# Performance work log

Measured on AMD Instinct MI355X. Metric: run time of the kernel, lower is better.

## Reference

```python
import jax, jax.numpy as jnp
import numpy as np

PLP_ORDER = 16
N_CHANNEL = 40
FFT_LENGTH = 512
SAMPLE_RATE = 16000
LIFTER = 22
COMP_FACTOR = 0.33
FLOOR = 1e-5
F_MIN = 0.0
F_MAX = SAMPLE_RATE / 2


def _hz_to_mel(hz):
    return 1127.0 * np.log1p(np.asarray(hz, dtype=np.float64) / 700.0)


def _mel_to_hz(mel):
    return 700.0 * np.expm1(np.asarray(mel, dtype=np.float64) / 1127.0)


def _build_constants():
    # SPTK-style mel filter bank (triangular in mel domain).
    mel_min = _hz_to_mel(F_MIN)
    mel_max = _hz_to_mel(F_MAX)
    lower_bin = max(1, int(F_MIN / SAMPLE_RATE * FFT_LENGTH + 1.5))
    upper_bin = min(FFT_LENGTH // 2, int(F_MAX / SAMPLE_RATE * FFT_LENGTH + 0.5))
    seed = np.arange(1, N_CHANNEL + 2)
    cf_mel = (mel_max - mel_min) / (N_CHANNEL + 1) * seed + mel_min  # (C+1,)
    bins = np.arange(lower_bin, upper_bin)
    mel = _hz_to_mel(SAMPLE_RATE * bins / FFT_LENGTH)
    ch = np.searchsorted(cf_mel, mel, side='left')  # first center freq >= mel
    diff = cf_mel - np.concatenate([[mel_min], cf_mel[:-1]])
    w = (cf_mel[ch] - mel) / diff[ch]
    H = np.zeros((len(bins), N_CHANNEL))
    rows = np.arange(len(bins))
    low = ch - 1
    m_lo = low >= 0
    H[rows[m_lo], low[m_lo]] += w[m_lo]
    m_hi = ch <= N_CHANNEL - 1
    H[rows[m_hi], ch[m_hi]] += 1.0 - w[m_hi]
    # Equal-loudness curve over the first C center frequencies (in Hz).
    cf_hz = _mel_to_hz(cf_mel)
    f2 = cf_hz[:N_CHANNEL] ** 2
    eql = (f2 / (f2 + 160000.0)) ** 2 * (f2 + 1440000.0) / (f2 + 9610000.0)
    # Liftering vector, v[0] = 2.
    m = np.arange(PLP_ORDER + 1)
    lift = 1.0 + LIFTER / 2.0 * np.sin(np.pi / LIFTER * m)
    lift[0] = 2.0
    return lower_bin, upper_bin, H.astype(np.float32), eql.astype(np.float32), lift.astype(np.float32)


LOWER_BIN, UPPER_BIN, H_NP, EQL_NP, LIFT_NP = _build_constants()


def _levinson_durbin(r):
    # r: (..., M+1) autocorrelation -> (gain K, LPC coefficients a_1..a_M)
    M = PLP_ORDER
    E = r[..., 0]
    a = jnp.zeros(r.shape[:-1] + (M,), r.dtype)
    for i in range(1, M + 1):
        acc = r[..., i]
        if i > 1:
            acc = acc + jnp.einsum('...j,...j->...', a[..., : i - 1], r[..., 1:i][..., ::-1])
        k = -acc / E
        if i > 1:
            a = a.at[..., : i - 1].set(a[..., : i - 1] + k[..., None] * a[..., : i - 1][..., ::-1])
        a = a.at[..., i - 1].set(k)
        E = E * (1.0 - k * k)
    return jnp.sqrt(E), a


def _lpc_to_cepstrum(K, a):
    # c0 = log K; c_m = -a_m - sum_{k=1}^{m-1} (k/m) c_k a_{m-k}
    M = PLP_ORDER
    c = [jnp.log(K)]
    for m in range(1, M + 1):
        acc = a[..., m - 1]
        for k in range(1, m):
            acc = acc + (k / m) * c[k] * a[..., m - k - 1]
        c.append(-acc)
    return jnp.stack(c, axis=-1)  # (..., M+1)


def _plp(x):
    H = jnp.asarray(H_NP)
    eql = jnp.asarray(EQL_NP)
    lift = jnp.asarray(LIFT_NP)
    # Mel filter bank on power spectrum (use_power=True)
    fb = jnp.matmul(x[..., LOWER_BIN:UPPER_BIN], H)          # (..., C)
    logfb = jnp.log(jnp.maximum(fb, FLOOR))
    # Equal-loudness scaling + cubic-root amplitude compression
    y = (jnp.exp(logfb) * eql) ** COMP_FACTOR                # (..., C)
    # replicate1: duplicate first and last channels
    y = jnp.concatenate([y[..., :1], y, y[..., -1:]], axis=-1)  # (..., C+2)
    n = y.shape[-1]
    # hfft with norm='forward' -> inverse-FFT-like autocorrelation
    r = jnp.fft.hfft(y) / (2 * (n - 1))
    r = r[..., : PLP_ORDER + 1]
    K, a = _levinson_durbin(r)
    c = _lpc_to_cepstrum(K, a)
    c = c * lift
    return c[..., 1:]  # out_format 'y': PLP without C0, (..., M)


def setup_inputs() -> dict:
    key = jax.random.key(0)
    x = jax.random.uniform(key, (32, 4096, FFT_LENGTH // 2 + 1), dtype=jnp.float32)
    return {"x": x}


def reference(x):
    return _plp(x)
```

## Files before the change

### kernel.cpp

```cpp
#include <hip/hip_runtime.h>

#define NCH   40
#define MORD  16
#define NR    17
#define NY    42
#define NBINS 257

namespace cfg {

constexpr double PI  = 3.14159265358979323846264338327950288;
constexpr double LN2 = 0.693147180559945309417232121458176568;

constexpr double cexp(double x) {
    double t = 1.0, s = 1.0;
    for (int i = 1; i < 40; ++i) { t *= x / i; s += t; }
    return s;
}

constexpr double clog(double z) {
    double lg = 0.0;
    while (z > 1.4142135623730951) { z *= 0.5; lg += LN2; }
    while (z < 0.7071067811865476) { z *= 2.0; lg -= LN2; }
    double u = (z - 1.0) / (z + 1.0), u2 = u * u, t = u, s = u;
    for (int k = 1; k < 24; ++k) { t *= u2; s += t / (2.0 * k + 1.0); }
    return lg + 2.0 * s;
}

constexpr double ccos(double x) {
    double tp = 2.0 * PI;
    double q = x / tp;
    long long k = (long long)(q + (q >= 0.0 ? 0.5 : -0.5));
    double r = x - (double)k * tp;
    double r2 = r * r, t = 1.0, s = 1.0;
    for (int i = 1; i < 20; ++i) { t *= -r2 / ((2.0 * i - 1.0) * (2.0 * i)); s += t; }
    return s;
}

constexpr double csin(double x) { return ccos(x - PI / 2.0); }

struct Tab {
    int   start[43];
    float w[257];
    float eql[NCH];
    float lift[NR];
    float ct[NR][NY];
    constexpr Tab() : start(), w(), eql(), lift(), ct() {
        const double lmax  = clog(87.0 / 7.0);
        const double U1127 = lmax / 41.0;
        for (int c = 0; c <= 42 - 1; ++c) {
            double thr = 22.4 * (cexp((double)c * U1127) - 1.0);
            int s = (int)thr + 1;
            if (s < 1) s = 1;
            if (s > 256) s = 256;
            start[c] = s;
        }
        start[42 - 1] = start[41];
        for (int c = 0; c <= 40; ++c) {
            for (int b = start[c]; b < start[c + 1]; ++b) {
                double mel = 1127.0 * clog(1.0 + (double)b * 31.25 / 700.0);
                double t   = mel / (1127.0 * U1127);
                w[b] = (float)(t - (double)c);
            }
        }
        for (int c = 0; c < NCH; ++c) {
            double cf = 700.0 * (cexp((double)(c + 1) * U1127) - 1.0);
            double f2 = cf * cf;
            double e  = f2 / (f2 + 160000.0);
            e = e * e * (f2 + 1440000.0) / (f2 + 9610000.0);
            eql[c] = (float)e;
        }
        for (int m = 0; m < NR; ++m)
            lift[m] = (float)(1.0 + 11.0 * csin(PI * (double)m / 22.0));
        lift[0] = 2.0f;
        for (int l = 0; l < NR; ++l)
            for (int j = 0; j < NY; ++j) {
                double s = (j == 0 || j == NY - 1) ? 1.0 : 2.0;
                ct[l][j] = (float)(s * ccos(PI * (double)(j * l) / 41.0) / 82.0);
            }
    }
};

constexpr Tab T{};

}

__global__ __launch_bounds__(256) void plp_kernel(const float* __restrict__ x,
                                                  float* __restrict__ out,
                                                  int nframes)
{
    using cfg::T;
    const long long frame = (long long)blockIdx.x * blockDim.x + threadIdx.x;
    if (frame >= nframes) return;
    const float* __restrict__ xf = x + frame * NBINS;

    float fb[NCH];
    #pragma unroll
    for (int c = 0; c < NCH; ++c) fb[c] = 0.f;

    #pragma unroll
    for (int c = 0; c <= 40; ++c) {
        #pragma unroll
        for (int b = T.start[c]; b < T.start[c + 1]; ++b) {
            float xv = xf[b];
            const float wa = T.w[b];
            if (c < 40) fb[c]     = fmaf(wa, xv, fb[c]);
            if (c >= 1) fb[c - 1] = fmaf(1.0f - wa, xv, fb[c - 1]);
        }
    }

    float ys[NY];
    #pragma unroll
    for (int c = 0; c < NCH; ++c) {
        float v = fmaxf(fb[c], 1e-5f) * T.eql[c];
        ys[c + 1] = __expf(0.33f * __logf(v));
    }
    ys[0] = ys[1];
    ys[NY - 1] = ys[NY - 2];

    float r[NR];
    #pragma unroll
    for (int l = 0; l < NR; ++l) {
        float acc = 0.f;
        #pragma unroll
        for (int j = 0; j < NY; ++j) acc = fmaf(T.ct[l][j], ys[j], acc);
        r[l] = acc;
    }

    float a[MORD];
    #pragma unroll
    for (int i = 0; i < MORD; ++i) a[i] = 0.f;
    float E = r[0];
    #pragma unroll
    for (int i = 1; i <= MORD; ++i) {
        float acc = r[i];
        #pragma unroll
        for (int j = 0; j < i - 1; ++j) acc = fmaf(a[j], r[i - 1 - j], acc);
        float k = -acc / E;
        const int half = (i - 1) / 2;
        #pragma unroll
        for (int j = 0; j < half; ++j) {
            float t1 = a[j], t2 = a[i - 2 - j];
            a[j]         = fmaf(k, t2, t1);
            a[i - 2 - j] = fmaf(k, t1, t2);
        }
        if ((i - 1) & 1) a[half] = fmaf(k, a[half], a[half]);
        a[i - 1] = k;
        E = E * (1.f - k * k);
    }

    float cc[NR];
    #pragma unroll
    for (int m = 1; m <= MORD; ++m) {
        float acc = a[m - 1];
        #pragma unroll
        for (int k2 = 1; k2 < m; ++k2)
            acc = fmaf(((float)k2 / (float)m) * cc[k2], a[m - k2 - 1], acc);
        cc[m] = -acc;
    }

    float o[16];
    #pragma unroll
    for (int m = 1; m <= MORD; ++m) o[m - 1] = cc[m] * T.lift[m];

    float4* op = reinterpret_cast<float4*>(out + (size_t)frame * 16);
    op[0] = make_float4(o[0],  o[1],  o[2],  o[3]);
    op[1] = make_float4(o[4],  o[5],  o[6],  o[7]);
    op[2] = make_float4(o[8],  o[9],  o[10], o[11]);
    op[3] = make_float4(o[12], o[13], o[14], o[15]);
}

extern "C" void kernel_launch(void* const* d_in, const int* in_sizes, int n_in,
                              void* d_out, int out_size, void* d_ws, size_t ws_size,
                              hipStream_t stream) {
    const float* x   = (const float*)d_in[0];
    float*      outp = (float*)d_out;
    int nframes = in_sizes[0] / NBINS;
    int nblocks = (nframes + 255) / 256;
    plp_kernel<<<nblocks, 256, 0, stream>>>(x, outp, nframes);
}
```

Before: 221.3 us.

## Stage frame spectra into LDS with coalesced direct global-to-LDS loads

Each block of 64 frames now copies its contiguous 64x257-float slab into shared memory with global_load_lds 16-byte transfers, so consecutive lanes read consecutive addresses. Threads then read their own frame from LDS. Before, each thread walked its own frame with a 1028-byte stride, which gave poorly coalesced global reads. In exchange the block size drops from 256 to 64 and each block uses about 66 KB of LDS. That limits occupancy, and the per-thread LDS reads at stride 257 may hit bank conflicts.

```diff
diff --git a/kernel.cpp b/kernel.cpp
--- a/kernel.cpp
+++ b/kernel.cpp
@@ -5,6 +5,7 @@
 #define NR    17
 #define NY    42
 #define NBINS 257
+#define FPB   64
 
 namespace cfg {
 
@@ -47,7 +48,7 @@
     constexpr Tab() : start(), w(), eql(), lift(), ct() {
         const double lmax  = clog(87.0 / 7.0);
         const double U1127 = lmax / 41.0;
-        for (int c = 0; c <= 42 - 1; ++c) {
+        for (int c = 0; c <= 41; ++c) {
             double thr = 22.4 * (cexp((double)c * U1127) - 1.0);
             int s = (int)thr + 1;
             if (s < 1) s = 1;
@@ -84,14 +85,34 @@
 
 }
 
-__global__ __launch_bounds__(256) void plp_kernel(const float* __restrict__ x,
+__global__ __launch_bounds__(FPB) void plp_kernel(const float* __restrict__ x,
                                                   float* __restrict__ out,
                                                   int nframes)
 {
     using cfg::T;
-    const long long frame = (long long)blockIdx.x * blockDim.x + threadIdx.x;
+    __shared__ float slab[FPB * NBINS];
+    const int tid = threadIdx.x;
+    const long long F0 = (long long)blockIdx.x * FPB;
+
+    {
+        const float* base = x + F0 * NBINS + tid * 4;
+        const float* gend = x + (long long)nframes * NBINS;
+        #pragma unroll
+        for (int k = 0; k < 65; ++k) {
+            const int off = (k < 64) ? k * 256 : (FPB * NBINS - 256);
+            const float* src = base + off;
+            if (src + 4 > gend) src = gend - 4;
+            __builtin_amdgcn_global_load_lds(
+                (const __attribute__((address_space(1))) void*)src,
+                (__attribute__((address_space(3))) void*)(slab + off),
+                16, 0, 0);
+        }
+    }
+    __syncthreads();
+
+    const long long frame = F0 + tid;
     if (frame >= nframes) return;
-    const float* __restrict__ xf = x + frame * NBINS;
+    const float* __restrict__ fr = slab + tid * NBINS;
 
     float fb[NCH];
     #pragma unroll
@@ -101,7 +122,7 @@
     for (int c = 0; c <= 40; ++c) {
         #pragma unroll
         for (int b = T.start[c]; b < T.start[c + 1]; ++b) {
-            float xv = xf[b];
+            float xv = fr[b];
             const float wa = T.w[b];
             if (c < 40) fb[c]     = fmaf(wa, xv, fb[c]);
             if (c >= 1) fb[c - 1] = fmaf(1.0f - wa, xv, fb[c - 1]);
@@ -175,6 +196,6 @@
     const float* x   = (const float*)d_in[0];
     float*      outp = (float*)d_out;
     int nframes = in_sizes[0] / NBINS;
-    int nblocks = (nframes + 255) / 256;
-    plp_kernel<<<nblocks, 256, 0, stream>>>(x, outp, nframes);
-}
+    int nblocks = (nframes + FPB - 1) / FPB;
+    plp_kernel<<<nblocks, FPB, 0, stream>>>(x, outp, nframes);
+}
```

After: 204.6 us. -7.6%, faster.

## Stage frame slabs through LDS with coalesced float4 loads

Applied to the files above, without the earlier changes.

Each block now cooperatively loads 64 frames (about 64 KB) into shared memory using all 256 threads with coalesced float4 reads, and only the first 64 threads then compute one frame each from LDS. This replaces the strided per-thread global reads, where consecutive threads touched addresses 1 KB apart. The Levinson division is also replaced with a hardware reciprocal. The trade-offs are that three quarters of the threads sit idle during compute, and the large LDS footprint limits occupancy to roughly two blocks per CU. The float4 loads also depend on 64*257 floats being 16-byte aligned.

```diff
diff --git a/kernel.cpp b/kernel.cpp
--- a/kernel.cpp
+++ b/kernel.cpp
@@ -1,10 +1,13 @@
 #include <hip/hip_runtime.h>
 
-#define NCH   40
-#define MORD  16
-#define NR    17
-#define NY    42
-#define NBINS 257
+#define NCH    40
+#define MORD   16
+#define NR     17
+#define NY     42
+#define NBINS  257
+#define FPB    64
+#define SLABF  (FPB * NBINS)
+#define NF4    (SLABF / 4)
 
 namespace cfg {
 
@@ -47,7 +50,7 @@
     constexpr Tab() : start(), w(), eql(), lift(), ct() {
         const double lmax  = clog(87.0 / 7.0);
         const double U1127 = lmax / 41.0;
-        for (int c = 0; c <= 42 - 1; ++c) {
+        for (int c = 0; c <= 41; ++c) {
             double thr = 22.4 * (cexp((double)c * U1127) - 1.0);
             int s = (int)thr + 1;
             if (s < 1) s = 1;
@@ -89,19 +92,42 @@
                                                   int nframes)
 {
     using cfg::T;
-    const long long frame = (long long)blockIdx.x * blockDim.x + threadIdx.x;
+    __shared__ float slab[SLABF];
+    const int tid = threadIdx.x;
+    const long long F0 = (long long)blockIdx.x * FPB;
+
+    {
+        const float4* gsrc = reinterpret_cast<const float4*>(x + F0 * NBINS);
+        float4* lsdst = reinterpret_cast<float4*>(slab);
+        const long long maxf4 = ((long long)nframes * NBINS) / 4 - F0 * NBINS / 4;
+        #pragma unroll
+        for (int r = 0; r < 16; ++r) {
+            int i = r * 256 + tid;
+            long long ii = (i < maxf4) ? i : (maxf4 - 1);
+            lsdst[i] = gsrc[ii];
+        }
+        if (tid < NF4 - 4096) {
+            int i = 4096 + tid;
+            long long ii = (i < maxf4) ? i : (maxf4 - 1);
+            lsdst[i] = gsrc[ii];
+        }
+    }
+    __syncthreads();
+
+    if (tid >= FPB) return;
+
+    const long long frame = F0 + tid;
     if (frame >= nframes) return;
-    const float* __restrict__ xf = x + frame * NBINS;
+    const float* fr = slab + tid * NBINS;
 
     float fb[NCH];
     #pragma unroll
     for (int c = 0; c < NCH; ++c) fb[c] = 0.f;
-
     #pragma unroll
     for (int c = 0; c <= 40; ++c) {
         #pragma unroll
         for (int b = T.start[c]; b < T.start[c + 1]; ++b) {
-            float xv = xf[b];
+            float xv = fr[b];
             const float wa = T.w[b];
             if (c < 40) fb[c]     = fmaf(wa, xv, fb[c]);
             if (c >= 1) fb[c - 1] = fmaf(1.0f - wa, xv, fb[c - 1]);
@@ -135,7 +161,7 @@
         float acc = r[i];
         #pragma unroll
         for (int j = 0; j < i - 1; ++j) acc = fmaf(a[j], r[i - 1 - j], acc);
-        float k = -acc / E;
+        float k = -acc * __builtin_amdgcn_rcpf(E);
         const int half = (i - 1) / 2;
         #pragma unroll
         for (int j = 0; j < half; ++j) {
@@ -175,6 +201,6 @@
     const float* x   = (const float*)d_in[0];
     float*      outp = (float*)d_out;
     int nframes = in_sizes[0] / NBINS;
-    int nblocks = (nframes + 255) / 256;
+    int nblocks = (nframes + FPB - 1) / FPB;
     plp_kernel<<<nblocks, 256, 0, stream>>>(x, outp, nframes);
 }
```

After: 203.9 us. 1.09x faster.
